# Kernel optimization log

Hardware: AMD Instinct MI355X
Metric: run time of the kernel (lower is better)

## Reference

```python
import jax, jax.numpy as jnp
import numpy as np

D_MODEL = 128
N_HEADS = 8
D_K = D_MODEL // N_HEADS
N_NODES = 50000
N_EDGES = 800000


def setup_inputs() -> dict:
    key = jax.random.key(0)
    ks = jax.random.split(key, 8)
    X = jax.random.normal(ks[0], (N_NODES, D_MODEL), dtype=jnp.float32)
    nbr_src = jax.random.randint(ks[1], (N_EDGES,), 0, N_NODES, dtype=jnp.int32)
    nbr_dst = jax.random.randint(ks[2], (N_EDGES,), 0, N_NODES, dtype=jnp.int32)
    s = 1.0 / np.sqrt(D_MODEL)
    W_qkv = jax.random.normal(ks[3], (3 * D_MODEL, D_MODEL), dtype=jnp.float32) * s
    w_bias = jax.random.normal(ks[4], (N_HEADS, D_MODEL), dtype=jnp.float32) * s
    W_gate = jax.random.normal(ks[5], (D_MODEL, D_MODEL), dtype=jnp.float32) * s
    b_gate = jax.random.normal(ks[6], (D_MODEL,), dtype=jnp.float32) * s
    W_o = jax.random.normal(ks[7], (D_MODEL, D_MODEL), dtype=jnp.float32) * s
    return {"X": X, "W_qkv": W_qkv, "w_bias": w_bias, "W_gate": W_gate,
            "b_gate": b_gate, "W_o": W_o, "nbr_src": nbr_src,
            "nbr_dst": nbr_dst, "num_cells": N_NODES}


def segment_softmax(scores, seg, num_segments):
    # scores: [E, H], seg: [E] -> softmax over edges sharing the same seg id
    mx = jax.ops.segment_max(scores, seg, num_segments=num_segments)  # [N, H]
    mx = jnp.where(jnp.isfinite(mx), mx, -1e9)
    exp_s = jnp.exp(scores - mx[seg])
    sm = jax.ops.segment_sum(exp_s, seg, num_segments=num_segments)  # [N, H]
    return exp_s / (sm[seg] + 1e-12)


def reference(X, W_qkv, w_bias, W_gate, b_gate, W_o, nbr_src, nbr_dst, num_cells):
    H, dk = N_HEADS, D_K
    scale = 1.0 / np.sqrt(dk)
    qkv = (X @ W_qkv.T).reshape(-1, 3, H, dk)      # [N, 3, H, dk]
    Q, K, V = qkv[:, 0], qkv[:, 1], qkv[:, 2]
    gate = jax.nn.sigmoid(X @ W_gate.T + b_gate).reshape(-1, H, dk)
    bias = X @ w_bias.T                             # [N, H]
    scores = jnp.einsum('ehd,ehd->eh', Q[nbr_src], K[nbr_dst]) * scale + bias[nbr_src]
    attn = segment_softmax(scores, nbr_src, num_cells)          # [E, H]
    out = jax.ops.segment_sum(attn[:, :, None] * V[nbr_dst], nbr_src,
                              num_segments=num_cells)           # [N, H, dk]
    return (gate * out).reshape(-1, D_MODEL) @ W_o.T
```

## Files before the change

### kernel.cpp

```cpp
#include <hip/hip_runtime.h>
#include <hip/hip_fp16.h>

#define DM 128
#define NHEADS 8
#define MAXDEG 64
#define SROW 136

typedef _Float16 half8 __attribute__((ext_vector_type(8)));
typedef float floatx4 __attribute__((ext_vector_type(4)));

__global__ __launch_bounds__(256) void build_w16(const float* __restrict__ Wqkv,
    const float* __restrict__ Wgate, const float* __restrict__ wbias,
    const float* __restrict__ Wo, _Float16* __restrict__ Wcat16, _Float16* __restrict__ Wo16) {
  int i = blockIdx.x * 256 + threadIdx.x;
  if (i < 576 * 128) {
    int r = i >> 7;
    float v;
    if (r < 384) v = Wqkv[i];
    else if (r < 512) v = Wgate[i - 384 * 128];
    else if (r < 520) v = wbias[i - 512 * 128];
    else v = 0.f;
    Wcat16[i] = (_Float16)v;
  } else if (i < 576 * 128 + 128 * 128) {
    int j = i - 576 * 128;
    Wo16[j] = (_Float16)Wo[j];
  }
}

__global__ __launch_bounds__(256) void proj_gemm_mfma(
    const float* __restrict__ X, const _Float16* __restrict__ W,
    const float* __restrict__ b_gate,
    _Float16* __restrict__ Q, _Float16* __restrict__ KV,
    _Float16* __restrict__ gate, float* __restrict__ bias, int M) {
  __shared__ _Float16 As[128 * SROW];
  __shared__ _Float16 Bs[64 * SROW];
  int tid = threadIdx.x;
  int m0 = blockIdx.x * 128;

#pragma unroll
  for (int i = 0; i < 4; i++) {
    int u = tid + i * 256;
    int r = u >> 3;
    int cc = (u & 7) * 16;
    int gr = m0 + r;
    float4 f0, f1, f2, f3;
    if (gr < M) {
      const float4* src = (const float4*)(X + (size_t)gr * 128 + cc);
      f0 = src[0]; f1 = src[1]; f2 = src[2]; f3 = src[3];
    } else {
      f0 = f1 = f2 = f3 = make_float4(0.f, 0.f, 0.f, 0.f);
    }
    half8 h0 = {(_Float16)f0.x, (_Float16)f0.y, (_Float16)f0.z, (_Float16)f0.w,
                (_Float16)f1.x, (_Float16)f1.y, (_Float16)f1.z, (_Float16)f1.w};
    half8 h1 = {(_Float16)f2.x, (_Float16)f2.y, (_Float16)f2.z, (_Float16)f2.w,
                (_Float16)f3.x, (_Float16)f3.y, (_Float16)f3.z, (_Float16)f3.w};
    *(half8*)(As + r * SROW + cc) = h0;
    *(half8*)(As + r * SROW + cc + 8) = h1;
  }

  int wid = tid >> 6, lane = tid & 63;
  int quad = lane >> 4, l16 = lane & 15;
  int mw = wid * 32;

  for (int c = 0; c < 9; c++) {
    __syncthreads();
#pragma unroll
    for (int i = 0; i < 4; i++) {
      int u = tid + i * 256;
      int r = u >> 4;
      int cc = (u & 15) * 8;
      *(int4*)(Bs + r * SROW + cc) = *(const int4*)(W + (size_t)(c * 64 + r) * 128 + cc);
    }
    __syncthreads();

    floatx4 acc[2][4] = {};
#pragma unroll
    for (int kc = 0; kc < 4; kc++) {
      int ko = kc * 32 + quad * 8;
      half8 a0 = *(const half8*)(As + (mw + l16) * SROW + ko);
      half8 a1 = *(const half8*)(As + (mw + 16 + l16) * SROW + ko);
      half8 b[4];
#pragma unroll
      for (int ni = 0; ni < 4; ni++)
        b[ni] = *(const half8*)(Bs + (ni * 16 + l16) * SROW + ko);
#pragma unroll
      for (int ni = 0; ni < 4; ni++) {
        acc[0][ni] = __builtin_amdgcn_mfma_f32_16x16x32_f16(a0, b[ni], acc[0][ni], 0, 0, 0);
        acc[1][ni] = __builtin_amdgcn_mfma_f32_16x16x32_f16(a1, b[ni], acc[1][ni], 0, 0, 0);
      }
    }

    if (c == 8) {
      if (l16 < 8) {
#pragma unroll
        for (int mi = 0; mi < 2; mi++)
#pragma unroll
          for (int r = 0; r < 4; r++) {
            int row = m0 + mw + mi * 16 + quad * 4 + r;
            if (row < M) bias[(size_t)row * 8 + l16] = acc[mi][0][r];
          }
      }
    } else {
      int reg = c >> 1;
#pragma unroll
      for (int mi = 0; mi < 2; mi++) {
#pragma unroll
        for (int ni = 0; ni < 4; ni++) {
          int colL = (c & 1) * 64 + ni * 16 + l16;
#pragma unroll
          for (int r = 0; r < 4; r++) {
            int row = m0 + mw + mi * 16 + quad * 4 + r;
            if (row >= M) continue;
            float v = acc[mi][ni][r];
            if (reg == 0)      Q[(size_t)row * 128 + colL] = (_Float16)v;
            else if (reg == 1) KV[(size_t)row * 256 + colL] = (_Float16)v;
            else if (reg == 2) KV[(size_t)row * 256 + 128 + colL] = (_Float16)v;
            else gate[(size_t)row * 128 + colL] =
                   (_Float16)(1.0f / (1.0f + __expf(-(v + b_gate[colL]))));
          }
        }
      }
    }
  }
}

__global__ __launch_bounds__(256) void final_gemm_mfma(
    const _Float16* __restrict__ A, const _Float16* __restrict__ W,
    float* __restrict__ C, int M) {
  __shared__ _Float16 As[128 * SROW];
  __shared__ _Float16 Bs[64 * SROW];
  int tid = threadIdx.x;
  int m0 = blockIdx.x * 128, n0 = blockIdx.y * 64;
#pragma unroll
  for (int i = 0; i < 8; i++) {
    int u = tid + i * 256;
    int r = u >> 4;
    int cc = (u & 15) * 8;
    int gr = m0 + r;
    int4 val = make_int4(0, 0, 0, 0);
    if (gr < M) val = *(const int4*)(A + (size_t)gr * 128 + cc);
    *(int4*)(As + r * SROW + cc) = val;
  }
#pragma unroll
  for (int i = 0; i < 4; i++) {
    int u = tid + i * 256;
    int r = u >> 4;
    int cc = (u & 15) * 8;
    *(int4*)(Bs + r * SROW + cc) = *(const int4*)(W + (size_t)(n0 + r) * 128 + cc);
  }
  __syncthreads();

  int wid = tid >> 6, lane = tid & 63;
  int quad = lane >> 4, l16 = lane & 15;
  int mw = (wid >> 1) * 64;
  int nw = (wid & 1) * 32;

  floatx4 acc[4][2] = {};
#pragma unroll
  for (int kc = 0; kc < 4; kc++) {
    int ko = kc * 32 + quad * 8;
    half8 a[4], b[2];
#pragma unroll
    for (int mi = 0; mi < 4; mi++)
      a[mi] = *(const half8*)(As + (mw + mi * 16 + l16) * SROW + ko);
#pragma unroll
    for (int ni = 0; ni < 2; ni++)
      b[ni] = *(const half8*)(Bs + (nw + ni * 16 + l16) * SROW + ko);
#pragma unroll
    for (int mi = 0; mi < 4; mi++)
#pragma unroll
      for (int ni = 0; ni < 2; ni++)
        acc[mi][ni] = __builtin_amdgcn_mfma_f32_16x16x32_f16(a[mi], b[ni], acc[mi][ni], 0, 0, 0);
  }
#pragma unroll
  for (int mi = 0; mi < 4; mi++) {
#pragma unroll
    for (int ni = 0; ni < 2; ni++) {
      int col = n0 + nw + ni * 16 + l16;
#pragma unroll
      for (int r = 0; r < 4; r++) {
        int row = m0 + mw + mi * 16 + quad * 4 + r;
        if (row >= M) continue;
        C[(size_t)row * 128 + col] = acc[mi][ni][r];
      }
    }
  }
}

__global__ __launch_bounds__(256) void build_csr(const int* __restrict__ src_idx,
    const int* __restrict__ dst_idx, int* __restrict__ cnt,
    int* __restrict__ csr_dst, int E) {
  int e = blockIdx.x * 256 + threadIdx.x;
  if (e >= E) return;
  int s = src_idx[e];
  int d = dst_idx[e];
  int p = atomicAdd(&cnt[s], 1);
  if (p < MAXDEG) csr_dst[(size_t)s * MAXDEG + p] = d;
}

__global__ __launch_bounds__(256) void attn_fused(
    const int* __restrict__ cnt, const int* __restrict__ csr_dst,
    const _Float16* __restrict__ Q, const _Float16* __restrict__ KV,
    const float* __restrict__ bias, const _Float16* __restrict__ gate,
    _Float16* __restrict__ gated, int N) {
  int wave = threadIdx.x >> 6, lane = threadIdx.x & 63;
  int n = blockIdx.x * 4 + wave;
  if (n >= N) return;
  int deg = cnt[n];
  if (deg > MAXDEG) deg = MAXDEG;
  int qtr = lane >> 4, l16 = lane & 15;
  int ch0 = l16 * 8;

  int dstv = csr_dst[(size_t)n * MAXDEG + lane];

  half8 qv = *(const half8*)(Q + (size_t)n * DM + ch0);
  float qf[8];
#pragma unroll
  for (int j = 0; j < 8; j++) qf[j] = (float)qv[j];
  float bias_h = bias[(size_t)n * NHEADS + (l16 >> 1)];

  float acc[8] = {};
  float den = 0.f;
  int iters = (deg + 3) >> 2;

  half8 kc = {}, vc = {};
  bool valc = qtr < deg;
  {
    int d = __shfl(dstv, qtr);
    d = valc ? d : 0;
    const _Float16* kvp = KV + (size_t)d * 256 + ch0;
    kc = *(const half8*)(kvp);
    vc = *(const half8*)(kvp + 128);
  }
  for (int it = 0; it < iters; it++) {
    half8 kn = {}, vn = {};
    bool valn = false;
    if (it + 1 < iters) {
      int ein = (it + 1) * 4 + qtr;
      valn = ein < deg;
      int d = __shfl(dstv, ein);
      d = valn ? d : 0;
      const _Float16* kvp = KV + (size_t)d * 256 + ch0;
      kn = *(const half8*)(kvp);
      vn = *(const half8*)(kvp + 128);
    }
    float p = 0.f;
#pragma unroll
    for (int j = 0; j < 8; j++) p += qf[j] * (float)kc[j];
    p += __shfl_xor(p, 1);
    float w = __expf(p * 0.25f + bias_h);
    if (!valc) w = 0.f;
    den += w;
#pragma unroll
    for (int j = 0; j < 8; j++) acc[j] = fmaf(w, (float)vc[j], acc[j]);
    kc = kn; vc = vn; valc = valn;
  }
#pragma unroll
  for (int j = 0; j < 8; j++) acc[j] += __shfl_xor(acc[j], 16);
#pragma unroll
  for (int j = 0; j < 8; j++) acc[j] += __shfl_xor(acc[j], 32);
  den += __shfl_xor(den, 16);
  den += __shfl_xor(den, 32);

  if (qtr == 0) {
    float inv = 1.0f / (den + 1e-12f);
    half8 gv = *(const half8*)(gate + (size_t)n * DM + ch0);
    half8 o;
#pragma unroll
    for (int j = 0; j < 8; j++) o[j] = (_Float16)(acc[j] * inv * (float)gv[j]);
    *(half8*)(gated + (size_t)n * DM + ch0) = o;
  }
}

extern "C" void kernel_launch(void* const* d_in, const int* in_sizes, int n_in,
                              void* d_out, int out_size, void* d_ws, size_t ws_size,
                              hipStream_t stream) {
  const float* X     = (const float*)d_in[0];
  const float* Wqkv  = (const float*)d_in[1];
  const float* wbias = (const float*)d_in[2];
  const float* Wgate = (const float*)d_in[3];
  const float* bgate = (const float*)d_in[4];
  const float* Wo    = (const float*)d_in[5];
  const int*   nsrc  = (const int*)d_in[6];
  const int*   ndst  = (const int*)d_in[7];
  int N = in_sizes[0] / 128;
  int E = in_sizes[6];
  float* out = (float*)d_out;

  char* p = (char*)d_ws;
  _Float16* Wcat16  = (_Float16*)p; p += 576 * 128 * sizeof(_Float16);
  _Float16* Wo16    = (_Float16*)p; p += 128 * 128 * sizeof(_Float16);
  _Float16* Q16     = (_Float16*)p; p += (size_t)N * 128 * sizeof(_Float16);
  _Float16* KV16    = (_Float16*)p; p += (size_t)N * 256 * sizeof(_Float16);
  _Float16* gate16  = (_Float16*)p; p += (size_t)N * 128 * sizeof(_Float16);
  _Float16* gated16 = (_Float16*)p; p += (size_t)N * 128 * sizeof(_Float16);
  float* bias       = (float*)p;    p += (size_t)N * 8 * sizeof(float);
  int* cnt          = (int*)p;      p += (size_t)N * sizeof(int);
  int* csr_dst      = (int*)p;      p += (size_t)N * MAXDEG * sizeof(int);

  hipMemsetAsync(cnt, 0, (size_t)N * sizeof(int), stream);

  build_w16<<<(576 * 128 + 128 * 128 + 255) / 256, 256, 0, stream>>>(
      Wqkv, Wgate, wbias, Wo, Wcat16, Wo16);

  build_csr<<<(E + 255) / 256, 256, 0, stream>>>(nsrc, ndst, cnt, csr_dst, E);

  proj_gemm_mfma<<<(N + 127) / 128, 256, 0, stream>>>(
      X, Wcat16, bgate, Q16, KV16, gate16, bias, N);

  attn_fused<<<(N + 3) / 4, 256, 0, stream>>>(cnt, csr_dst, Q16, KV16, bias,
                                              gate16, gated16, N);

  dim3 fg((N + 127) / 128, 2);
  final_gemm_mfma<<<fg, 256, 0, stream>>>(gated16, Wo16, out, N);
}
```

Baseline: 239.3 us.

## Fuse weight conversion and CSR build into projection kernel, deepen attention prefetch

Drops the separate weight fp16 conversion kernel by converting fp32 weights on the fly inside both GEMM tile loads, and merges the CSR build into the projection launch as extra blocks so the two run concurrently. The attention kernel now prefetches two edge groups ahead instead of one and uses packed fp16 dot2 for the QK score. This cuts two kernel launches and overlaps the atomic-bound CSR work with the GEMM, at the cost of redundant per-block weight conversion and more registers in the attention loop.

```diff
diff --git a/kernel.cpp b/kernel.cpp
--- a/kernel.cpp
+++ b/kernel.cpp
@@ -7,35 +7,47 @@
 #define SROW 136
 
 typedef _Float16 half8 __attribute__((ext_vector_type(8)));
+typedef _Float16 half2v __attribute__((ext_vector_type(2)));
 typedef float floatx4 __attribute__((ext_vector_type(4)));
 
-__global__ __launch_bounds__(256) void build_w16(const float* __restrict__ Wqkv,
+union H8 { half8 v; half2v h2[4]; };
+
+__global__ __launch_bounds__(256) void proj_csr(
+    const float* __restrict__ X, const float* __restrict__ Wqkv,
     const float* __restrict__ Wgate, const float* __restrict__ wbias,
-    const float* __restrict__ Wo, _Float16* __restrict__ Wcat16, _Float16* __restrict__ Wo16) {
-  int i = blockIdx.x * 256 + threadIdx.x;
-  if (i < 576 * 128) {
-    int r = i >> 7;
-    float v;
-    if (r < 384) v = Wqkv[i];
-    else if (r < 512) v = Wgate[i - 384 * 128];
-    else if (r < 520) v = wbias[i - 512 * 128];
-    else v = 0.f;
-    Wcat16[i] = (_Float16)v;
-  } else if (i < 576 * 128 + 128 * 128) {
-    int j = i - 576 * 128;
-    Wo16[j] = (_Float16)Wo[j];
-  }
-}
-
-__global__ __launch_bounds__(256) void proj_gemm_mfma(
-    const float* __restrict__ X, const _Float16* __restrict__ W,
     const float* __restrict__ b_gate,
+    const int* __restrict__ nsrc, const int* __restrict__ ndst,
+    int* __restrict__ cnt, int* __restrict__ csr_dst,
     _Float16* __restrict__ Q, _Float16* __restrict__ KV,
-    _Float16* __restrict__ gate, float* __restrict__ bias, int M) {
+    _Float16* __restrict__ gate, float* __restrict__ bias,
+    int M, int E, int P) {
   __shared__ _Float16 As[128 * SROW];
   __shared__ _Float16 Bs[64 * SROW];
   int tid = threadIdx.x;
-  int m0 = blockIdx.x * 128;
+  int bid = blockIdx.x;
+
+  if (bid >= P) {
+    int ebase = (bid - P) * 8192;
+    for (int g = 0; g < 4; g++) {
+      int s[8], d[8];
+#pragma unroll
+      for (int j = 0; j < 8; j++) {
+        int e = ebase + (g * 8 + j) * 256 + tid;
+        s[j] = (e < E) ? nsrc[e] : -1;
+        d[j] = (e < E) ? ndst[e] : 0;
+      }
+#pragma unroll
+      for (int j = 0; j < 8; j++) {
+        if (s[j] >= 0) {
+          int p = atomicAdd(&cnt[s[j]], 1);
+          if (p < MAXDEG) csr_dst[(size_t)s[j] * MAXDEG + p] = d[j];
+        }
+      }
+    }
+    return;
+  }
+
+  int m0 = bid * 128;
 
 #pragma unroll
   for (int i = 0; i < 4; i++) {
@@ -69,7 +81,19 @@
       int u = tid + i * 256;
       int r = u >> 4;
       int cc = (u & 15) * 8;
-      *(int4*)(Bs + r * SROW + cc) = *(const int4*)(W + (size_t)(c * 64 + r) * 128 + cc);
+      int grow = c * 64 + r;
+      const float* src = nullptr;
+      if (grow < 384)      src = Wqkv + (size_t)grow * 128 + cc;
+      else if (grow < 512) src = Wgate + (size_t)(grow - 384) * 128 + cc;
+      else if (grow < 520) src = wbias + (size_t)(grow - 512) * 128 + cc;
+      half8 h = {};
+      if (src) {
+        float4 f0 = ((const float4*)src)[0];
+        float4 f1 = ((const float4*)src)[1];
+        h = half8{(_Float16)f0.x, (_Float16)f0.y, (_Float16)f0.z, (_Float16)f0.w,
+                  (_Float16)f1.x, (_Float16)f1.y, (_Float16)f1.z, (_Float16)f1.w};
+      }
+      *(half8*)(Bs + r * SROW + cc) = h;
     }
     __syncthreads();
 
@@ -125,7 +149,7 @@
 }
 
 __global__ __launch_bounds__(256) void final_gemm_mfma(
-    const _Float16* __restrict__ A, const _Float16* __restrict__ W,
+    const _Float16* __restrict__ A, const float* __restrict__ Wo,
     float* __restrict__ C, int M) {
   __shared__ _Float16 As[128 * SROW];
   __shared__ _Float16 Bs[64 * SROW];
@@ -146,7 +170,12 @@
     int u = tid + i * 256;
     int r = u >> 4;
     int cc = (u & 15) * 8;
-    *(int4*)(Bs + r * SROW + cc) = *(const int4*)(W + (size_t)(n0 + r) * 128 + cc);
+    const float* src = Wo + (size_t)(n0 + r) * 128 + cc;
+    float4 f0 = ((const float4*)src)[0];
+    float4 f1 = ((const float4*)src)[1];
+    half8 h = {(_Float16)f0.x, (_Float16)f0.y, (_Float16)f0.z, (_Float16)f0.w,
+               (_Float16)f1.x, (_Float16)f1.y, (_Float16)f1.z, (_Float16)f1.w};
+    *(half8*)(Bs + r * SROW + cc) = h;
   }
   __syncthreads();
 
@@ -185,17 +214,6 @@
       }
     }
   }
-}
-
-__global__ __launch_bounds__(256) void build_csr(const int* __restrict__ src_idx,
-    const int* __restrict__ dst_idx, int* __restrict__ cnt,
-    int* __restrict__ csr_dst, int E) {
-  int e = blockIdx.x * 256 + threadIdx.x;
-  if (e >= E) return;
-  int s = src_idx[e];
-  int d = dst_idx[e];
-  int p = atomicAdd(&cnt[s], 1);
-  if (p < MAXDEG) csr_dst[(size_t)s * MAXDEG + p] = d;
 }
 
 __global__ __launch_bounds__(256) void attn_fused(
@@ -213,47 +231,60 @@
 
   int dstv = csr_dst[(size_t)n * MAXDEG + lane];
 
-  half8 qv = *(const half8*)(Q + (size_t)n * DM + ch0);
-  float qf[8];
-#pragma unroll
-  for (int j = 0; j < 8; j++) qf[j] = (float)qv[j];
+  H8 qu; qu.v = *(const half8*)(Q + (size_t)n * DM + ch0);
   float bias_h = bias[(size_t)n * NHEADS + (l16 >> 1)];
 
   float acc[8] = {};
   float den = 0.f;
   int iters = (deg + 3) >> 2;
 
-  half8 kc = {}, vc = {};
-  bool valc = qtr < deg;
-  {
-    int d = __shfl(dstv, qtr);
-    d = valc ? d : 0;
+  H8 k0, v0, k1, v1;
+  k0.v = half8{}; v0.v = half8{}; k1.v = half8{}; v1.v = half8{};
+  bool b0 = false, b1 = false;
+  if (0 < iters) {
+    int e = qtr;
+    b0 = e < deg;
+    int d = __shfl(dstv, e);
+    d = b0 ? d : 0;
     const _Float16* kvp = KV + (size_t)d * 256 + ch0;
-    kc = *(const half8*)(kvp);
-    vc = *(const half8*)(kvp + 128);
-  }
+    k0.v = *(const half8*)kvp;
+    v0.v = *(const half8*)(kvp + 128);
+  }
+  if (1 < iters) {
+    int e = 4 + qtr;
+    b1 = e < deg;
+    int d = __shfl(dstv, e);
+    d = b1 ? d : 0;
+    const _Float16* kvp = KV + (size_t)d * 256 + ch0;
+    k1.v = *(const half8*)kvp;
+    v1.v = *(const half8*)(kvp + 128);
+  }
+
   for (int it = 0; it < iters; it++) {
-    half8 kn = {}, vn = {};
-    bool valn = false;
-    if (it + 1 < iters) {
-      int ein = (it + 1) * 4 + qtr;
-      valn = ein < deg;
-      int d = __shfl(dstv, ein);
-      d = valn ? d : 0;
+    H8 k2, v2;
+    k2.v = half8{}; v2.v = half8{};
+    bool b2 = false;
+    if (it + 2 < iters) {
+      int e = (it + 2) * 4 + qtr;
+      b2 = e < deg;
+      int d = __shfl(dstv, e);
+      d = b2 ? d : 0;
       const _Float16* kvp = KV + (size_t)d * 256 + ch0;
-      kn = *(const half8*)(kvp);
-      vn = *(const half8*)(kvp + 128);
+      k2.v = *(const half8*)kvp;
+      v2.v = *(const half8*)(kvp + 128);
     }
     float p = 0.f;
 #pragma unroll
-    for (int j = 0; j < 8; j++) p += qf[j] * (float)kc[j];
+    for (int j = 0; j < 4; j++)
+      p = __builtin_amdgcn_fdot2(qu.h2[j], k0.h2[j], p, false);
     p += __shfl_xor(p, 1);
     float w = __expf(p * 0.25f + bias_h);
-    if (!valc) w = 0.f;
+    if (!b0) w = 0.f;
     den += w;
 #pragma unroll
-    for (int j = 0; j < 8; j++) acc[j] = fmaf(w, (float)vc[j], acc[j]);
-    kc = kn; vc = vn; valc = valn;
+    for (int j = 0; j < 8; j++) acc[j] = fmaf(w, (float)v0.v[j], acc[j]);
+    k0 = k1; v0 = v1; b0 = b1;
+    k1 = k2; v1 = v2; b1 = b2;
   }
 #pragma unroll
   for (int j = 0; j < 8; j++) acc[j] += __shfl_xor(acc[j], 16);
@@ -288,8 +319,6 @@
   float* out = (float*)d_out;
 
   char* p = (char*)d_ws;
-  _Float16* Wcat16  = (_Float16*)p; p += 576 * 128 * sizeof(_Float16);
-  _Float16* Wo16    = (_Float16*)p; p += 128 * 128 * sizeof(_Float16);
   _Float16* Q16     = (_Float16*)p; p += (size_t)N * 128 * sizeof(_Float16);
   _Float16* KV16    = (_Float16*)p; p += (size_t)N * 256 * sizeof(_Float16);
   _Float16* gate16  = (_Float16*)p; p += (size_t)N * 128 * sizeof(_Float16);
@@ -300,17 +329,14 @@
 
   hipMemsetAsync(cnt, 0, (size_t)N * sizeof(int), stream);
 
-  build_w16<<<(576 * 128 + 128 * 128 + 255) / 256, 256, 0, stream>>>(
-      Wqkv, Wgate, wbias, Wo, Wcat16, Wo16);
-
-  build_csr<<<(E + 255) / 256, 256, 0, stream>>>(nsrc, ndst, cnt, csr_dst, E);
-
-  proj_gemm_mfma<<<(N + 127) / 128, 256, 0, stream>>>(
-      X, Wcat16, bgate, Q16, KV16, gate16, bias, N);
+  int P = (N + 127) / 128;
+  int C = (E + 8191) / 8192;
+  proj_csr<<<P + C, 256, 0, stream>>>(X, Wqkv, Wgate, wbias, bgate, nsrc, ndst,
+                                      cnt, csr_dst, Q16, KV16, gate16, bias, N, E, P);
 
   attn_fused<<<(N + 3) / 4, 256, 0, stream>>>(cnt, csr_dst, Q16, KV16, bias,
                                               gate16, gated16, N);
 
   dim3 fg((N + 127) / 128, 2);
-  final_gemm_mfma<<<fg, 256, 0, stream>>>(gated16, Wo16, out, N);
+  final_gemm_mfma<<<fg, 256, 0, stream>>>(gated16, Wo, out, N);
 }
```

Result: faster. 217.4 us (-9.1%).
